# Kernel optimization log

Measured on AMD Instinct MI355X. Metric: run time of the kernel, lower is better.

Reference implementation:

```python
import jax, jax.numpy as jnp
import numpy as np

N, D, H, DH, E = 50000, 128, 4, 32, 600000
EPS = 1e-5


def _seg_softmax(logits, seg, n):
    # numerically stable softmax over edges grouped by destination node
    m = jax.ops.segment_max(logits, seg, num_segments=n)
    e = jnp.exp(logits - m[seg])
    s = jax.ops.segment_sum(e, seg, num_segments=n)
    return e / s[seg]


def _bn(x, g, b):
    # BatchNorm1d, training-mode statistics (biased variance), eps=1e-5
    mu = jnp.mean(x, 0)
    var = jnp.mean((x - mu) ** 2, 0)
    return g * (x - mu) * jax.lax.rsqrt(var + EPS) + b


def _gat(x, src, dst, W, a_s, a_d, bias):
    # PyG GATConv: shared lin, additive attention, leaky_relu(0.2), dst-softmax, concat heads + bias
    n = x.shape[0]
    xp = (x @ W).reshape(n, H, DH)
    al_s = jnp.sum(xp * a_s, -1)  # [N,H]
    al_d = jnp.sum(xp * a_d, -1)
    lg = jax.nn.leaky_relu(al_s[src] + al_d[dst], 0.2)  # [E',H]
    alpha = _seg_softmax(lg, dst, n)
    out = jax.ops.segment_sum(alpha[..., None] * xp[src], dst, num_segments=n)
    return out.reshape(n, H * DH) + bias


def setup_inputs() -> dict:
    key = jax.random.key(0)
    ks = jax.random.split(key, 24)
    s = 0.05
    inp = {
        'x_cell': jax.random.normal(ks[0], (N, D), jnp.float32),
        'z_h': jax.random.normal(ks[1], (D,), jnp.float32),
        'x_cell_embedded': jax.random.normal(ks[2], (N, D), jnp.float32),
        'edge_index_0': jax.random.randint(ks[3], (2, E), 0, N, dtype=jnp.int32),
        'edge_index_1': jax.random.randint(ks[4], (2, E), 0, N, dtype=jnp.int32),
        # GAT params, stacked over (conv layer 0/1, edge type 0/1)
        'gat_W': jax.random.normal(ks[5], (2, 2, D, D), jnp.float32) * s,
        'gat_att_src': jax.random.normal(ks[6], (2, 2, H, DH), jnp.float32) * s,
        'gat_att_dst': jax.random.normal(ks[7], (2, 2, H, DH), jnp.float32) * s,
        'gat_bias': jnp.zeros((2, 2, D), jnp.float32),
        # BatchNorm params for bn1, bn2, bn_hgt
        'bn_gamma': jnp.ones((3, D), jnp.float32),
        'bn_beta': jnp.zeros((3, D), jnp.float32),
        # HGTConv params
        'hgt_Wk': jax.random.normal(ks[8], (D, D), jnp.float32) * s,
        'hgt_bk': jnp.zeros((D,), jnp.float32),
        'hgt_Wq': jax.random.normal(ks[9], (D, D), jnp.float32) * s,
        'hgt_bq': jnp.zeros((D,), jnp.float32),
        'hgt_Wv': jax.random.normal(ks[10], (D, D), jnp.float32) * s,
        'hgt_bv': jnp.zeros((D,), jnp.float32),
        'hgt_a_rel': jax.random.normal(ks[11], (2, H, DH, DH), jnp.float32) * s,
        'hgt_m_rel': jax.random.normal(ks[12], (2, H, DH, DH), jnp.float32) * s,
        'hgt_p_rel': jnp.ones((2, H), jnp.float32),
        'hgt_Wo': jax.random.normal(ks[13], (D, D), jnp.float32) * s,
        'hgt_bo': jnp.zeros((D,), jnp.float32),
        'hgt_skip': jnp.float32(1.0),
        # input injection + FiLM
        'inj_W': jax.random.normal(ks[14], (D, D), jnp.float32) * s,
        'inj_b': jnp.zeros((D,), jnp.float32),
        'film_W1': jax.random.normal(ks[15], (D, 2 * D), jnp.float32) * s,
        'film_b1': jnp.zeros((2 * D,), jnp.float32),
        'film_W2': jax.random.normal(ks[16], (2 * D, 2 * D), jnp.float32) * s,
        'film_b2': jnp.zeros((2 * D,), jnp.float32),
    }
    return inp


def reference(x_cell, z_h, x_cell_embedded, edge_index_0, edge_index_1,
              gat_W, gat_att_src, gat_att_dst, gat_bias, bn_gamma, bn_beta,
              hgt_Wk, hgt_bk, hgt_Wq, hgt_bq, hgt_Wv, hgt_bv,
              hgt_a_rel, hgt_m_rel, hgt_p_rel, hgt_Wo, hgt_bo, hgt_skip,
              inj_W, inj_b, film_W1, film_b1, film_W2, film_b2):
    n = x_cell.shape[0]
    loops = jnp.arange(n, dtype=edge_index_0.dtype)
    # GATConv add_self_loops=True: augment each relation's edge list with self loops
    eis = [(jnp.concatenate([ei[0], loops]), jnp.concatenate([ei[1], loops]))
           for ei in (edge_index_0, edge_index_1)]

    def hetero_gat(x, c):
        out = jnp.zeros((n, D), x.dtype)
        for t, (src, dst) in enumerate(eis):  # HeteroConv aggr='sum'
            out = out + _gat(x, src, dst, gat_W[c, t], gat_att_src[c, t], gat_att_dst[c, t], gat_bias[c, t])
        return out

    lrelu = lambda v: jax.nn.leaky_relu(v, 0.2)
    x1 = lrelu(x_cell + _bn(hetero_gat(x_cell, 0), bn_gamma[0], bn_beta[0]))
    x2 = lrelu(x1 + _bn(hetero_gat(x1, 1), bn_gamma[1], bn_beta[1]))

    # HGTConv (single node type, 2 edge types, no self loops)
    k = (x2 @ hgt_Wk + hgt_bk).reshape(n, H, DH)
    q = (x2 @ hgt_Wq + hgt_bq).reshape(n, H, DH)
    v = (x2 @ hgt_Wv + hgt_bv).reshape(n, H, DH)
    lgs, msgs, dsts = [], [], []
    inv_sqrt = np.float32(1.0 / np.sqrt(DH))
    for t, ei in enumerate((edge_index_0, edge_index_1)):
        src, dst = ei[0], ei[1]
        kt = jnp.einsum('nhd,hde->nhe', k, hgt_a_rel[t])  # relation-transformed keys
        vt = jnp.einsum('nhd,hde->nhe', v, hgt_m_rel[t])  # relation-transformed values
        lgs.append(jnp.sum(q[dst] * kt[src], -1) * hgt_p_rel[t] * inv_sqrt)  # [E,H]
        msgs.append(vt[src])
        dsts.append(dst)
    lg = jnp.concatenate(lgs)
    msg = jnp.concatenate(msgs)
    dst_all = jnp.concatenate(dsts)
    alpha = _seg_softmax(lg, dst_all, n)  # softmax over all incoming edges (all relations)
    agg = jax.ops.segment_sum(alpha[..., None] * msg, dst_all, num_segments=n).reshape(n, H * DH)
    hgt_out = jax.nn.gelu(agg, approximate=False) @ hgt_Wo + hgt_bo
    sk = jax.nn.sigmoid(hgt_skip)
    x3 = sk * hgt_out + (1.0 - sk) * x2

    x3 = _bn(x3, bn_gamma[2], bn_beta[2])
    x3 = lrelu(x2 + x3)
    x3 = x3 + x_cell_embedded @ inj_W + inj_b

    # FiLM on global z_h
    hzh = jax.nn.gelu(z_h @ film_W1 + film_b1, approximate=False)
    gb = hzh @ film_W2 + film_b2
    gamma, beta = gb[:D], gb[D:]
    return gamma * x3 + beta
```

## Files before the change

### kernel.cpp

```cpp
#include <hip/hip_runtime.h>
#include <math.h>

#define NN 50000
#define DD 128
#define HH 4
#define DHH 32
#define EE 600000
#define N2 (2*NN)
#define NBLK 256

typedef unsigned short u16;
typedef unsigned int   u32;
typedef unsigned char  u8;
using short8 = __attribute__((ext_vector_type(8))) short;
using f32x4  = __attribute__((ext_vector_type(4))) float;
using f32x2  = __attribute__((ext_vector_type(2))) float;

#define LOG2E 1.44269504f

__device__ __forceinline__ float lrelu(float v){ return v > 0.f ? v : 0.2f*v; }
__device__ __forceinline__ float gelu_exact(float x){ return 0.5f*x*(1.f+erff(x*0.70710678118654752f)); }
__device__ __forceinline__ u16 f2bf(float f){
  u32 u = __float_as_uint(f);
  u32 r = (u + 0x7fffu + ((u>>16)&1u)) >> 16;
  return (u16)r;
}
__device__ __forceinline__ u32 pack2bf(float a, float b){ return (u32)f2bf(a) | ((u32)f2bf(b)<<16); }
__device__ __forceinline__ float bflo(u32 u){ return __uint_as_float(u<<16); }
__device__ __forceinline__ float bfhi(u32 u){ return __uint_as_float(u & 0xffff0000u); }

__global__ __launch_bounds__(256) void prep_all(
    const float* __restrict__ gat_W, const float* __restrict__ Wk, const float* __restrict__ Wv,
    const float* __restrict__ Wo, const float* __restrict__ injW, u16* __restrict__ WT,
    const float* __restrict__ Wq, const float* __restrict__ bq, const float* __restrict__ a_rel,
    u16* __restrict__ wqtT, float* __restrict__ bqt,
    const float* __restrict__ z, const float* __restrict__ fW1, const float* __restrict__ fb1,
    const float* __restrict__ fW2, const float* __restrict__ fb2, float* __restrict__ gb){
  __shared__ float t[32][33];
  __shared__ float hsh[256];
  const int bid = blockIdx.x;
  if(bid < 128){
    const int m = bid >> 4, tile = bid & 15, tr = tile>>2, tc = tile&3;
    const float* src = (m<4) ? (gat_W + (size_t)m*16384) : (m==4? Wk : m==5? Wv : m==6? Wo : injW);
    const int lr = threadIdx.x>>5, lc = threadIdx.x&31;
    #pragma unroll
    for(int p=0;p<4;++p) t[lr+p*8][lc] = src[(size_t)(tr*32+lr+p*8)*128 + tc*32+lc];
    __syncthreads();
    #pragma unroll
    for(int p=0;p<4;++p)
      WT[(size_t)m*16384 + (size_t)(tc*32+lr+p*8)*128 + tr*32+lc] = f2bf(t[lc][lr+p*8]);
  } else if(bid < 257){
    int idx = (bid-128)*256 + threadIdx.x;
    if(idx < 2*128*129){
      int tt = idx / (128*129);
      int r = idx % (128*129);
      int f = r / 129, c = r % 129;
      int h = f>>5, m = f&31;
      const float* srcp = (c<128) ? (Wq + (size_t)c*128 + h*DHH) : (bq + h*DHH);
      const float* arow = a_rel + (((size_t)(tt*HH+h)*DHH)+m)*DHH;
      float s=0.f;
      #pragma unroll
      for(int e=0;e<DHH;++e) s = fmaf(srcp[e], arow[e], s);
      if(c<128) wqtT[(size_t)tt*16384 + (size_t)f*128 + c] = f2bf(s);
      else      bqt[tt*128 + f] = s;
    }
  } else {
    int j = threadIdx.x;
    float acc = fb1[j];
    for(int d=0; d<DD; ++d) acc = fmaf(z[d], fW1[d*256+j], acc);
    hsh[j] = gelu_exact(acc);
    __syncthreads();
    float acc2 = fb2[j];
    for(int k=0;k<256;++k) acc2 = fmaf(hsh[k], fW2[k*256+j], acc2);
    gb[j] = acc2;
  }
}

__global__ void count2_kernel(const int* __restrict__ d0, const int* __restrict__ d1, int* __restrict__ jcnt){
  int e = blockIdx.x*blockDim.x+threadIdx.x;
  if(e < EE)        atomicAdd(&jcnt[d0[e]], 1);
  else if(e < 2*EE) atomicAdd(&jcnt[NN + d1[e-EE]], 1);
}

__global__ void scan_partial(const int* __restrict__ cnt, int* __restrict__ bsum){
  int t = threadIdx.x;
  int i0 = blockIdx.x*512 + 2*t;
  int s = 0;
  if(i0   < N2) s += cnt[i0];
  if(i0+1 < N2) s += cnt[i0+1];
  __shared__ int red[256];
  red[t]=s; __syncthreads();
  for(int off=128; off>0; off>>=1){ if(t<off) red[t]+=red[t+off]; __syncthreads(); }
  if(t==0) bsum[blockIdx.x]=red[0];
}

__global__ void scan_final2(const int* __restrict__ cnt, const int* __restrict__ bsum,
                            int* __restrict__ jrs, int* __restrict__ jcur, int nb){
  __shared__ int sh[256];
  int t = threadIdx.x;
  {
    int v = (t<nb)? bsum[t] : 0;
    sh[t]=v; __syncthreads();
    for(int off=1; off<256; off<<=1){
      int u = (t>=off)? sh[t-off] : 0; __syncthreads();
      sh[t]+=u; __syncthreads();
    }
  }
  const int bofsv = sh[blockIdx.x] - bsum[blockIdx.x];
  if(blockIdx.x==0 && t==0) jrs[N2] = sh[nb-1];
  __syncthreads();
  int i0 = blockIdx.x*512 + 2*t;
  int a = (i0   < N2)? cnt[i0]   : 0;
  int c = (i0+1 < N2)? cnt[i0+1] : 0;
  int s = a+c;
  sh[t]=s; __syncthreads();
  for(int off=1; off<256; off<<=1){
    int u = (t>=off)? sh[t-off] : 0; __syncthreads();
    sh[t]+=u; __syncthreads();
  }
  int ex = bofsv + sh[t]-s;
  if(i0   < N2){ jrs[i0]=ex;     jcur[i0]=ex; }
  if(i0+1 < N2){ jrs[i0+1]=ex+a; jcur[i0+1]=ex+a; }
}

__global__ void fill2_kernel(const int* __restrict__ ei0, const int* __restrict__ ei1,
                             int* __restrict__ jcur, u16* __restrict__ es){
  int e = blockIdx.x*blockDim.x+threadIdx.x;
  if(e < EE){
    int d = ei0[EE+e];
    int pos = atomicAdd(&jcur[d],1);
    es[pos] = (u16)ei0[e];
  } else if(e < 2*EE){
    int i = e-EE;
    int d = ei1[EE+i];
    int pos = atomicAdd(&jcur[NN+d],1);
    es[pos] = (u16)ei1[i];
  }
}

constexpr int MM_BIAS  = 1;
constexpr int MM_FILM  = 2;
constexpr int MM_SKIP  = 4;
constexpr int MM_ABF16 = 64;

#define SWZ(row, byte) ((byte) ^ (((row)&7)<<4))

template<int MODE>
__device__ __forceinline__ void mgemm_core(const void* Av, const u16* WT, int row0, int n,
                                           u16* Al, u16* Wl, f32x4 (&acc)[8]){
  const int tid = threadIdx.x;
  if(MODE & MM_ABF16){
    const uint2* Ag = (const uint2*)((const u16*)Av + (size_t)row0*128);
    const int maxv = (min(64, n-row0))*32;
    #pragma unroll
    for(int j=0;j<8;++j){
      int v = tid + j*256;
      uint2 st = make_uint2(0u,0u);
      if(v < maxv) st = Ag[v];
      int row = v>>5, cb = (v&31)*8;
      *(uint2*)((char*)Al + row*256 + SWZ(row, cb)) = st;
    }
  } else {
    const float4* Ag = (const float4*)((const float*)Av + (size_t)row0*128);
    const int maxv = (min(64, n-row0))*32;
    #pragma unroll
    for(int j=0;j<8;++j){
      int v = tid + j*256;
      float4 val = make_float4(0.f,0.f,0.f,0.f);
      if(v < maxv) val = Ag[v];
      int row = v>>5, cb = (v&31)*8;
      uint2 st; st.x = pack2bf(val.x, val.y); st.y = pack2bf(val.z, val.w);
      *(uint2*)((char*)Al + row*256 + SWZ(row, cb)) = st;
    }
  }
  {
    const u32* Wg = (const u32*)WT;
    #pragma unroll
    for(int j=0;j<32;++j){
      int v = tid + j*256;
      u32 w = Wg[v];
      int row = v>>6, cb = (v&63)*4;
      *(u32*)((char*)Wl + row*256 + SWZ(row, cb)) = w;
    }
  }
  __syncthreads();
  const int lane = tid & 63;
  const int wv   = tid >> 6;
  const int r16  = lane & 15;
  const int kg   = lane >> 4;
  #pragma unroll
  for(int nn=0;nn<8;++nn) acc[nn] = (f32x4){0.f,0.f,0.f,0.f};
  #pragma unroll
  for(int s=0;s<4;++s){
    const int arow = wv*16 + r16;
    const int kb = s*64 + kg*16;
    short8 af = *(const short8*)((const char*)Al + arow*256 + SWZ(arow, kb));
    #pragma unroll
    for(int nn=0;nn<8;++nn){
      const int brow = nn*16 + r16;
      short8 bf = *(const short8*)((const char*)Wl + brow*256 + SWZ(brow, kb));
      acc[nn] = __builtin_amdgcn_mfma_f32_16x16x32_bf16(af, bf, acc[nn], 0, 0, 0);
    }
  }
}

template<int MODE>
__global__ __launch_bounds__(256) void mgemm(const void* __restrict__ Av, const u16* __restrict__ WT,
    const float* __restrict__ bias, const float* __restrict__ base, const float* __restrict__ fgb,
    const float* __restrict__ skipv, float* __restrict__ C, int n){
  __shared__ u16 Al[64*128];
  __shared__ u16 Wl[128*128];
  const int row0 = blockIdx.x*64;
  f32x4 acc[8];
  mgemm_core<MODE>(Av, WT, row0, n, Al, Wl, acc);
  const int lane = threadIdx.x & 63;
  const int wv   = threadIdx.x >> 6;
  const int r16  = lane & 15;
  const int kg   = lane >> 4;
  float bvals[8];
  if(MODE & MM_BIAS){
    #pragma unroll
    for(int nn=0;nn<8;++nn) bvals[nn] = bias[nn*16+r16];
  }
  float sk = 0.f;
  if(MODE & MM_SKIP) sk = 1.f/(1.f+__expf(-skipv[0]));
  #pragma unroll
  for(int i=0;i<4;++i){
    const int row = row0 + wv*16 + kg*4 + i;
    if(row >= n) continue;
    #pragma unroll
    for(int nn=0;nn<8;++nn){
      const int col = nn*16 + r16;
      float o = acc[nn][i];
      if(MODE & MM_BIAS) o += bvals[nn];
      if(MODE & MM_SKIP)
        o = sk*o + (1.f-sk)*base[(size_t)row*128 + col];
      if(MODE & MM_FILM){
        o += base[(size_t)row*128 + col];
        o = fgb[col]*o + fgb[128+col];
      }
      C[(size_t)row*128 + col] = o;
    }
  }
}

struct MJob {
  const u16* WT;
  const float* bias;
  const float* as_;
  const float* ad_;
  void* Cv;
  int att_t;
  int sel;
};
struct MJobs { MJob j[4]; };

__global__ __launch_bounds__(256) void mgemmM(const float* __restrict__ Av, MJobs jobs, int njobs,
    float* __restrict__ als8, float* __restrict__ ald8, int n){
  __shared__ u16 Al[64*128];
  __shared__ u16 Wl[128*128];
  const int tid = threadIdx.x;
  const int row0 = blockIdx.x*64;
  {
    const float4* Ag = (const float4*)(Av + (size_t)row0*128);
    const int maxv = (min(64, n-row0))*32;
    #pragma unroll
    for(int j=0;j<8;++j){
      int v = tid + j*256;
      float4 val = make_float4(0.f,0.f,0.f,0.f);
      if(v < maxv) val = Ag[v];
      int row = v>>5, cb = (v&31)*8;
      uint2 st; st.x = pack2bf(val.x, val.y); st.y = pack2bf(val.z, val.w);
      *(uint2*)((char*)Al + row*256 + SWZ(row, cb)) = st;
    }
  }
  const int lane = tid & 63;
  const int wv   = tid >> 6;
  const int r16  = lane & 15;
  const int kg   = lane >> 4;
  for(int jj=0; jj<njobs; ++jj){
    const MJob job = jobs.j[jj];
    {
      const u32* Wg = (const u32*)job.WT;
      #pragma unroll
      for(int j=0;j<32;++j){
        int v = tid + j*256;
        u32 w = Wg[v];
        int row = v>>6, cb = (v&63)*4;
        *(u32*)((char*)Wl + row*256 + SWZ(row, cb)) = w;
      }
    }
    __syncthreads();
    f32x4 acc[8];
    #pragma unroll
    for(int nn=0;nn<8;++nn) acc[nn] = (f32x4){0.f,0.f,0.f,0.f};
    #pragma unroll
    for(int s=0;s<4;++s){
      const int arow = wv*16 + r16;
      const int kb = s*64 + kg*16;
      short8 af = *(const short8*)((const char*)Al + arow*256 + SWZ(arow, kb));
      #pragma unroll
      for(int nn=0;nn<8;++nn){
        const int brow = nn*16 + r16;
        short8 bf = *(const short8*)((const char*)Wl + brow*256 + SWZ(brow, kb));
        acc[nn] = __builtin_amdgcn_mfma_f32_16x16x32_bf16(af, bf, acc[nn], 0, 0, 0);
      }
    }
    if(job.as_){
      float asv[8], adv[8];
      #pragma unroll
      for(int nn=0;nn<8;++nn){ asv[nn]=job.as_[nn*16+r16]; adv[nn]=job.ad_[nn*16+r16]; }
      #pragma unroll
      for(int i=0;i<4;++i){
        const int row = row0 + wv*16 + kg*4 + i;
        #pragma unroll
        for(int h=0;h<4;++h){
          float ps = asv[2*h]*acc[2*h][i] + asv[2*h+1]*acc[2*h+1][i];
          float pd = adv[2*h]*acc[2*h][i] + adv[2*h+1]*acc[2*h+1][i];
          ps += __shfl_xor(ps,1); ps += __shfl_xor(ps,2); ps += __shfl_xor(ps,4); ps += __shfl_xor(ps,8);
          pd += __shfl_xor(pd,1); pd += __shfl_xor(pd,2); pd += __shfl_xor(pd,4); pd += __shfl_xor(pd,8);
          if(row < n && r16 == 0){
            als8[(size_t)row*8 + 2*h + job.att_t] = ps;
            ald8[(size_t)row*8 + 2*h + job.att_t] = pd;
          }
        }
      }
    }
    float bvals[8];
    #pragma unroll
    for(int nn=0;nn<8;++nn) bvals[nn] = job.bias ? job.bias[nn*16+r16] : 0.f;
    #pragma unroll
    for(int i=0;i<4;++i){
      const int row = row0 + wv*16 + kg*4 + i;
      if(row >= n) continue;
      #pragma unroll
      for(int nn=0;nn<8;++nn){
        const int col = nn*16 + r16;
        float o = acc[nn][i] + bvals[nn];
        if(job.sel == 1){
          ((u16*)job.Cv)[(size_t)row*128 + col] = f2bf(o);
        } else {
          u32 enc = __builtin_amdgcn_cvt_pk_fp8_f32(o, 0.f, 0u, false);
          ((u8*)job.Cv)[(size_t)row*256 + (col>>1)*4 + (col&1) + (job.sel-2)*2] = (u8)(enc & 0xffu);
        }
      }
    }
    __syncthreads();
  }
}

__global__ __launch_bounds__(256) void gat_gather3(const u16* __restrict__ xp0, const u16* __restrict__ xp1,
    const float* __restrict__ als8, const float* __restrict__ ald8,
    const int* __restrict__ jrs, const u16* __restrict__ es,
    const float* __restrict__ gb0, const float* __restrict__ gb1, float* __restrict__ out){
  const int gid = blockIdx.x*blockDim.x + threadIdx.x;
  const int node = gid >> 6;
  const int lane = threadIdx.x & 63;
  if(node >= NN) return;
  const int h = lane >> 4;
  const int cc = 2*lane;
  float o0 = gb0[cc] + gb1[cc], o1 = gb0[cc+1] + gb1[cc+1];
  #pragma unroll
  for(int t=0;t<2;++t){
    const u16* __restrict__ xp = t ? xp1 : xp0;
    const float aldv = ald8[(size_t)node*8 + 2*h + t];
    const int s0 = jrs[t*NN+node], s1 = jrs[t*NN+node+1];
    float ssum=0.f, a0=0.f, a1=0.f;
    int p = s0;
    for(; p+3<s1; p+=4){
      const int sA = es[p], sB = es[p+1], sC = es[p+2], sD = es[p+3];
      const u32 xA = *(const u32*)&xp[(size_t)sA*DD + cc];
      const u32 xB = *(const u32*)&xp[(size_t)sB*DD + cc];
      const u32 xC = *(const u32*)&xp[(size_t)sC*DD + cc];
      const u32 xD = *(const u32*)&xp[(size_t)sD*DD + cc];
      float lA = als8[(size_t)sA*8 + 2*h + t] + aldv;
      float lB = als8[(size_t)sB*8 + 2*h + t] + aldv;
      float lC = als8[(size_t)sC*8 + 2*h + t] + aldv;
      float lD = als8[(size_t)sD*8 + 2*h + t] + aldv;
      const float eA = exp2f(lA>0.f ? lA*LOG2E : lA*(0.2f*LOG2E));
      const float eB = exp2f(lB>0.f ? lB*LOG2E : lB*(0.2f*LOG2E));
      const float eC = exp2f(lC>0.f ? lC*LOG2E : lC*(0.2f*LOG2E));
      const float eD = exp2f(lD>0.f ? lD*LOG2E : lD*(0.2f*LOG2E));
      ssum += (eA+eB)+(eC+eD);
      a0 = fmaf(eA, bflo(xA), a0); a1 = fmaf(eA, bfhi(xA), a1);
      a0 = fmaf(eB, bflo(xB), a0); a1 = fmaf(eB, bfhi(xB), a1);
      a0 = fmaf(eC, bflo(xC), a0); a1 = fmaf(eC, bfhi(xC), a1);
      a0 = fmaf(eD, bflo(xD), a0); a1 = fmaf(eD, bfhi(xD), a1);
    }
    for(; p<s1; ++p){
      const int sA = es[p];
      const u32 xA = *(const u32*)&xp[(size_t)sA*DD + cc];
      float lA = als8[(size_t)sA*8 + 2*h + t] + aldv;
      const float eA = exp2f(lA>0.f ? lA*LOG2E : lA*(0.2f*LOG2E));
      ssum += eA;
      a0 = fmaf(eA, bflo(xA), a0); a1 = fmaf(eA, bfhi(xA), a1);
    }
    {
      float lg = als8[(size_t)node*8 + 2*h + t] + aldv;
      const float ev = exp2f(lg>0.f ? lg*LOG2E : lg*(0.2f*LOG2E));
      ssum += ev;
      const u32 xr = *(const u32*)&xp[(size_t)node*DD + cc];
      a0 = fmaf(ev, bflo(xr), a0); a1 = fmaf(ev, bfhi(xr), a1);
    }
    const float inv = 1.f/ssum;
    o0 = fmaf(a0, inv, o0); o1 = fmaf(a1, inv, o1);
  }
  *(float2*)&out[(size_t)node*DD + cc] = make_float2(o0, o1);
}

__global__ __launch_bounds__(256) void bn_stats_fused(const float* __restrict__ X, float* __restrict__ part,
                               const float* __restrict__ gamma, const float* __restrict__ beta,
                               float* __restrict__ stat, int* __restrict__ counter){
  const int f = threadIdx.x & 127, rg = threadIdx.x>>7;
  float s=0.f, s2=0.f;
  for(int r = blockIdx.x*2+rg; r<NN; r += NBLK*2){
    float v = X[(size_t)r*DD+f]; s+=v; s2 = fmaf(v,v,s2);
  }
  __shared__ float ls[256], ls2[256];
  __shared__ int lastsh;
  ls[threadIdx.x]=s; ls2[threadIdx.x]=s2; __syncthreads();
  if(rg==0){
    part[blockIdx.x*256 + f]       = ls[f]+ls[128+f];
    part[blockIdx.x*256 + 128 + f] = ls2[f]+ls2[128+f];
  }
  __threadfence();
  if(threadIdx.x==0) lastsh = (atomicAdd(counter,1) == NBLK-1);
  __syncthreads();
  if(lastsh){
    __threadfence();
    float ss=0.f, ss2=0.f;
    #pragma unroll 8
    for(int bk=rg; bk<NBLK; bk+=2){
      ss  += part[bk*256 + f];
      ss2 += part[bk*256 + 128 + f];
    }
    __syncthreads();
    ls[threadIdx.x]=ss; ls2[threadIdx.x]=ss2;
    __syncthreads();
    if(rg==0){
      float S1 = ls[f]+ls[128+f], S2 = ls2[f]+ls2[128+f];
      float mu = S1/(float)NN;
      float var = S2/(float)NN - mu*mu;
      float rs = rsqrtf(var+1e-5f);
      stat[f]     = gamma[f]*rs;
      stat[128+f] = beta[f] - gamma[f]*rs*mu;
    }
    if(threadIdx.x==0) *counter = 0;
  }
}

__global__ void bn_apply_lrelu(const float* __restrict__ xprev, const float* __restrict__ acc,
                               const float* __restrict__ stat, float* __restrict__ out){
  int idx = blockIdx.x*blockDim.x+threadIdx.x;
  if(idx >= NN*64) return;
  int c = (2*idx) & 127;
  float2 x = ((const float2*)xprev)[idx];
  float2 a = ((const float2*)acc)[idx];
  float o0 = lrelu(x.x + fmaf(stat[c],   a.x, stat[128+c]));
  float o1 = lrelu(x.y + fmaf(stat[c+1], a.y, stat[128+c+1]));
  ((float2*)out)[idx] = make_float2(o0,o1);
}

__global__ __launch_bounds__(256) void hgt_merged2(const u16* __restrict__ qt,
    const u32* __restrict__ kv, const int* __restrict__ jrs, const u16* __restrict__ es,
    const float* __restrict__ p_rel, u16* __restrict__ Sv){
  const int gid = blockIdx.x*blockDim.x + threadIdx.x;
  const int node = gid >> 6;
  const int lane = threadIdx.x & 63;
  if(node >= NN) return;
  const int h = lane >> 4;
  float acc[2][2] = {{0.f,0.f},{0.f,0.f}};
  float ssum = 0.f;
  #pragma unroll
  for(int t=0;t<2;++t){
    const u32 qw = *(const u32*)&qt[(size_t)t*NN*DD + (size_t)node*DD + 2*lane];
    const float q0 = bflo(qw), q1 = bfhi(qw);
    const float scale2 = p_rel[t*HH+h]*(0.17677669529663687f*LOG2E);
    const int s0 = jrs[t*NN+node], s1 = jrs[t*NN+node+1];
    int p = s0;
    for(; p+3<s1; p+=4){
      const int sA = es[p], sB = es[p+1], sC = es[p+2], sD = es[p+3];
      const u32 wA = kv[(size_t)sA*64 + lane];
      const u32 wB = kv[(size_t)sB*64 + lane];
      const u32 wC = kv[(size_t)sC*64 + lane];
      const u32 wD = kv[(size_t)sD*64 + lane];
      f32x2 kA = __builtin_amdgcn_cvt_pk_f32_fp8(wA, false);
      f32x2 kB = __builtin_amdgcn_cvt_pk_f32_fp8(wB, false);
      f32x2 kC = __builtin_amdgcn_cvt_pk_f32_fp8(wC, false);
      f32x2 kD = __builtin_amdgcn_cvt_pk_f32_fp8(wD, false);
      f32x2 vA = __builtin_amdgcn_cvt_pk_f32_fp8(wA, true);
      f32x2 vB = __builtin_amdgcn_cvt_pk_f32_fp8(wB, true);
      f32x2 vC = __builtin_amdgcn_cvt_pk_f32_fp8(wC, true);
      f32x2 vD = __builtin_amdgcn_cvt_pk_f32_fp8(wD, true);
      float pA = q0*kA.x + q1*kA.y;
      float pB = q0*kB.x + q1*kB.y;
      float pC = q0*kC.x + q1*kC.y;
      float pD = q0*kD.x + q1*kD.y;
      pA += __shfl_xor(pA,1); pB += __shfl_xor(pB,1); pC += __shfl_xor(pC,1); pD += __shfl_xor(pD,1);
      pA += __shfl_xor(pA,2); pB += __shfl_xor(pB,2); pC += __shfl_xor(pC,2); pD += __shfl_xor(pD,2);
      pA += __shfl_xor(pA,4); pB += __shfl_xor(pB,4); pC += __shfl_xor(pC,4); pD += __shfl_xor(pD,4);
      pA += __shfl_xor(pA,8); pB += __shfl_xor(pB,8); pC += __shfl_xor(pC,8); pD += __shfl_xor(pD,8);
      const float eA=exp2f(pA*scale2), eB=exp2f(pB*scale2);
      const float eC=exp2f(pC*scale2), eD=exp2f(pD*scale2);
      ssum += (eA+eB)+(eC+eD);
      acc[t][0] = fmaf(eA, vA.x, acc[t][0]); acc[t][1] = fmaf(eA, vA.y, acc[t][1]);
      acc[t][0] = fmaf(eB, vB.x, acc[t][0]); acc[t][1] = fmaf(eB, vB.y, acc[t][1]);
      acc[t][0] = fmaf(eC, vC.x, acc[t][0]); acc[t][1] = fmaf(eC, vC.y, acc[t][1]);
      acc[t][0] = fmaf(eD, vD.x, acc[t][0]); acc[t][1] = fmaf(eD, vD.y, acc[t][1]);
    }
    for(; p<s1; ++p){
      const int sA = es[p];
      const u32 wA = kv[(size_t)sA*64 + lane];
      f32x2 kA = __builtin_amdgcn_cvt_pk_f32_fp8(wA, false);
      f32x2 vA = __builtin_amdgcn_cvt_pk_f32_fp8(wA, true);
      float pA = q0*kA.x + q1*kA.y;
      pA += __shfl_xor(pA,1); pA += __shfl_xor(pA,2); pA += __shfl_xor(pA,4); pA += __shfl_xor(pA,8);
      const float eA = exp2f(pA*scale2);
      ssum += eA;
      acc[t][0] = fmaf(eA, vA.x, acc[t][0]); acc[t][1] = fmaf(eA, vA.y, acc[t][1]);
    }
  }
  const float inv = ssum>0.f ? 1.f/ssum : 0.f;
  ((u32*)&Sv[(size_t)node*256 +       2*lane])[0] = pack2bf(acc[0][0]*inv, acc[0][1]*inv);
  ((u32*)&Sv[(size_t)node*256 + 128 + 2*lane])[0] = pack2bf(acc[1][0]*inv, acc[1][1]*inv);
}

__global__ __launch_bounds__(256) void mtransform_kernel(const u16* __restrict__ Sv, const float* __restrict__ m_rel,
                                                         u16* __restrict__ out){
  __shared__ float Msh[2*HH*DHH*DHH];
  for(int i=threadIdx.x;i<2*HH*DHH*DHH;i+=256) Msh[i]=m_rel[i];
  __syncthreads();
  int idx = blockIdx.x*blockDim.x + threadIdx.x;
  if(idx >= NN*DD) return;
  int node = idx>>7, f = idx&127, h = f>>5, e = f&31;
  const u16* s0p = &Sv[(size_t)node*256 + h*DHH];
  const u16* s1p = &Sv[(size_t)node*256 + 128 + h*DHH];
  const float* M0 = &Msh[(0*HH+h)*DHH*DHH + e];
  const float* M1 = &Msh[(1*HH+h)*DHH*DHH + e];
  float s = 0.f;
  #pragma unroll
  for(int d=0; d<DHH; d+=2){
    u32 w0 = *(const u32*)&s0p[d];
    u32 w1 = *(const u32*)&s1p[d];
    s = fmaf(bflo(w0), M0[d*DHH],     s);
    s = fmaf(bfhi(w0), M0[(d+1)*DHH], s);
    s = fmaf(bflo(w1), M1[d*DHH],     s);
    s = fmaf(bfhi(w1), M1[(d+1)*DHH], s);
  }
  out[idx] = f2bf(gelu_exact(s));
}

extern "C" void kernel_launch(void* const* d_in, const int* in_sizes, int n_in,
                              void* d_out, int out_size, void* d_ws, size_t ws_size,
                              hipStream_t stream){
  const float* x_cell = (const float*)d_in[0];
  const float* z_h    = (const float*)d_in[1];
  const float* x_emb  = (const float*)d_in[2];
  const int*   ei0    = (const int*)d_in[3];
  const int*   ei1    = (const int*)d_in[4];
  const float* gat_W  = (const float*)d_in[5];
  const float* gat_as = (const float*)d_in[6];
  const float* gat_ad = (const float*)d_in[7];
  const float* gat_b  = (const float*)d_in[8];
  const float* bn_g   = (const float*)d_in[9];
  const float* bn_b   = (const float*)d_in[10];
  const float* Wk = (const float*)d_in[11];
  const float* bk = (const float*)d_in[12];
  const float* Wq = (const float*)d_in[13];
  const float* bq = (const float*)d_in[14];
  const float* Wv = (const float*)d_in[15];
  const float* bv = (const float*)d_in[16];
  const float* a_rel = (const float*)d_in[17];
  const float* m_rel = (const float*)d_in[18];
  const float* p_rel = (const float*)d_in[19];
  const float* Wo = (const float*)d_in[20];
  const float* bo = (const float*)d_in[21];
  const float* skip = (const float*)d_in[22];
  const float* injW = (const float*)d_in[23];
  const float* injb = (const float*)d_in[24];
  const float* fW1 = (const float*)d_in[25];
  const float* fb1 = (const float*)d_in[26];
  const float* fW2 = (const float*)d_in[27];
  const float* fb2 = (const float*)d_in[28];

  constexpr size_t SLOT = (size_t)NN*DD;
  float* ws = (float*)d_ws;
  float* A    = ws;
  float* X2   = A + SLOT;
  float* als8 = X2 + SLOT;
  float* ald8 = als8 + (size_t)NN*8;
  float* bnpart = ald8 + (size_t)NN*8;
  float* bnstat = bnpart + 256*256;
  float* fgb    = bnstat + 256;
  float* bqt    = fgb + 256;
  u16* WT8  = (u16*)(bqt + 2*128);
  u16* WQT  = WT8 + (size_t)8*16384;
  u16* S    = WQT + (size_t)2*16384;
  u16* XP0  = S + (size_t)NN*256;
  u16* XP1  = XP0 + SLOT;
  u16* es   = XP1 + SLOT;
  int* jcnt = (int*)(es + (size_t)2*EE + 2);
  int* bnctr= jcnt + N2;
  int* jrs  = bnctr + 4;
  int* jcur = jrs + N2 + 2;
  int* bsum = jcur + N2;
  size_t needed = (size_t)((char*)(bsum + 256) - (char*)d_ws);
  if(ws_size < needed) return;

  u16* QT = (u16*)A;
  u16* MT = (u16*)A;
  u32* KV = (u32*)XP0;

  const int TB = 256;
  dim3 b(TB);
  const int gE2    = (2*EE + TB - 1)/TB;
  const int gND    = (NN*DD + TB - 1)/TB;
  const int gND2   = (NN*64 + TB - 1)/TB;
  const int gNodes = (NN + 3)/4;
  const int gMG    = (NN + 63)/64;
  const int gScan  = (N2 + 511)/512;

  prep_all<<<258, b, 0, stream>>>(gat_W, Wk, Wv, Wo, injW, WT8, Wq, bq, a_rel, WQT, bqt,
                                  z_h, fW1, fb1, fW2, fb2, fgb);

  hipMemsetAsync(jcnt, 0, (N2+4)*sizeof(int), stream);
  count2_kernel<<<gE2, b, 0, stream>>>(ei0+EE, ei1+EE, jcnt);
  scan_partial<<<gScan, b, 0, stream>>>(jcnt, bsum);
  scan_final2<<<gScan, b, 0, stream>>>(jcnt, bsum, jrs, jcur, gScan);
  fill2_kernel<<<gE2, b, 0, stream>>>(ei0, ei1, jcur, es);

  const float* xin = x_cell;
  for(int c=0;c<2;++c){
    MJobs gj{};
    for(int t=0;t<2;++t){
      gj.j[t].WT   = WT8 + (size_t)(c*2+t)*16384;
      gj.j[t].bias = nullptr;
      gj.j[t].as_  = gat_as + (size_t)(c*2+t)*HH*DHH;
      gj.j[t].ad_  = gat_ad + (size_t)(c*2+t)*HH*DHH;
      gj.j[t].Cv   = t? (void*)XP1 : (void*)XP0;
      gj.j[t].att_t = t;
      gj.j[t].sel  = 1;
    }
    mgemmM<<<gMG, b, 0, stream>>>(xin, gj, 2, als8, ald8, NN);
    gat_gather3<<<gNodes, b, 0, stream>>>(XP0, XP1, als8, ald8, jrs, es,
        gat_b + (size_t)(c*2+0)*DD, gat_b + (size_t)(c*2+1)*DD, A);
    bn_stats_fused<<<NBLK, b, 0, stream>>>(A, bnpart, bn_g + (size_t)c*DD, bn_b + (size_t)c*DD, bnstat, bnctr);
    bn_apply_lrelu<<<gND2, b, 0, stream>>>(xin, A, bnstat, X2);
    xin = X2;
  }
  float* x2 = X2;

  {
    MJobs hj{};
    hj.j[0] = { WQT,                   bqt,       nullptr, nullptr, (void*)QT,          0, 1 };
    hj.j[1] = { WQT + 16384,           bqt + 128, nullptr, nullptr, (void*)(QT + SLOT), 0, 1 };
    hj.j[2] = { WT8 + (size_t)4*16384, bk,        nullptr, nullptr, (void*)KV,          0, 2 };
    hj.j[3] = { WT8 + (size_t)5*16384, bv,        nullptr, nullptr, (void*)KV,          0, 3 };
    mgemmM<<<gMG, b, 0, stream>>>(x2, hj, 4, nullptr, nullptr, NN);
  }
  hgt_merged2<<<gNodes, b, 0, stream>>>(QT, KV, jrs, es, p_rel, S);
  mtransform_kernel<<<gND, b, 0, stream>>>(S, m_rel, MT);
  mgemm<MM_ABF16|MM_BIAS|MM_SKIP><<<gMG, b, 0, stream>>>(MT, WT8 + (size_t)6*16384, bo,
      x2, nullptr, skip, (float*)d_out, NN);
  bn_stats_fused<<<NBLK, b, 0, stream>>>((float*)d_out, bnpart, bn_g + 2*DD, bn_b + 2*DD, bnstat, bnctr);
  bn_apply_lrelu<<<gND2, b, 0, stream>>>(x2, (float*)d_out, bnstat, (float*)d_out);
  mgemm<MM_BIAS|MM_FILM><<<gMG, b, 0, stream>>>(x_emb, WT8 + (size_t)7*16384, injb,
      (float*)d_out, fgb, nullptr, (float*)d_out, NN);
}
```

Baseline: 760.6 us.

## Build destination CSR with two-level bucket sort instead of per-node global atomics

After: 1.634 ms. +114.8%, slower.

```diff
diff --git a/kernel.cpp b/kernel.cpp
--- a/kernel.cpp
+++ b/kernel.cpp
@@ -8,6 +8,7 @@
 #define EE 600000
 #define N2 (2*NN)
 #define NBLK 256
+#define NBUCK ((N2 + 511)/512)
 
 typedef unsigned short u16;
 typedef unsigned int   u32;
@@ -76,66 +77,79 @@
   }
 }
 
-__global__ void count2_kernel(const int* __restrict__ d0, const int* __restrict__ d1, int* __restrict__ jcnt){
+__global__ __launch_bounds__(256) void bucket_count(const int* __restrict__ d0, const int* __restrict__ d1,
+                                                    int* __restrict__ bcnt){
+  __shared__ int h[NBUCK];
+  for(int i=threadIdx.x;i<NBUCK;i+=256) h[i]=0;
+  __syncthreads();
+  const int e0 = blockIdx.x*4096 + threadIdx.x;
+  #pragma unroll
+  for(int j=0;j<16;++j){
+    int e = e0 + j*256;
+    if(e < EE)           atomicAdd(&h[d0[e]>>9], 1);
+    else if(e < 2*EE)    atomicAdd(&h[(NN + d1[e-EE])>>9], 1);
+  }
+  __syncthreads();
+  for(int i=threadIdx.x;i<NBUCK;i+=256){ int v=h[i]; if(v) atomicAdd(&bcnt[i], v); }
+}
+
+__global__ void bucket_scan(const int* __restrict__ bcnt, int* __restrict__ bbase, int* __restrict__ bcur){
+  __shared__ int sh[256];
+  int t=threadIdx.x;
+  int v = (t<NBUCK)? bcnt[t] : 0;
+  sh[t]=v; __syncthreads();
+  for(int off=1;off<256;off<<=1){
+    int u=(t>=off)?sh[t-off]:0; __syncthreads();
+    sh[t]+=u; __syncthreads();
+  }
+  if(t<NBUCK){ bbase[t]=sh[t]-v; bcur[t]=sh[t]-v; }
+  if(t==0) bbase[NBUCK] = 2*EE;
+}
+
+__global__ void fill_bucket(const int* __restrict__ ei0, const int* __restrict__ ei1,
+                            int* __restrict__ bcur, u32* __restrict__ eb){
   int e = blockIdx.x*blockDim.x+threadIdx.x;
-  if(e < EE)        atomicAdd(&jcnt[d0[e]], 1);
-  else if(e < 2*EE) atomicAdd(&jcnt[NN + d1[e-EE]], 1);
-}
-
-__global__ void scan_partial(const int* __restrict__ cnt, int* __restrict__ bsum){
-  int t = threadIdx.x;
-  int i0 = blockIdx.x*512 + 2*t;
-  int s = 0;
-  if(i0   < N2) s += cnt[i0];
-  if(i0+1 < N2) s += cnt[i0+1];
-  __shared__ int red[256];
-  red[t]=s; __syncthreads();
-  for(int off=128; off>0; off>>=1){ if(t<off) red[t]+=red[t+off]; __syncthreads(); }
-  if(t==0) bsum[blockIdx.x]=red[0];
-}
-
-__global__ void scan_final2(const int* __restrict__ cnt, const int* __restrict__ bsum,
-                            int* __restrict__ jrs, int* __restrict__ jcur, int nb){
-  __shared__ int sh[256];
-  int t = threadIdx.x;
-  {
-    int v = (t<nb)? bsum[t] : 0;
-    sh[t]=v; __syncthreads();
-    for(int off=1; off<256; off<<=1){
-      int u = (t>=off)? sh[t-off] : 0; __syncthreads();
-      sh[t]+=u; __syncthreads();
-    }
-  }
-  const int bofsv = sh[blockIdx.x] - bsum[blockIdx.x];
-  if(blockIdx.x==0 && t==0) jrs[N2] = sh[nb-1];
-  __syncthreads();
-  int i0 = blockIdx.x*512 + 2*t;
-  int a = (i0   < N2)? cnt[i0]   : 0;
-  int c = (i0+1 < N2)? cnt[i0+1] : 0;
-  int s = a+c;
-  sh[t]=s; __syncthreads();
-  for(int off=1; off<256; off<<=1){
-    int u = (t>=off)? sh[t-off] : 0; __syncthreads();
-    sh[t]+=u; __syncthreads();
-  }
-  int ex = bofsv + sh[t]-s;
-  if(i0   < N2){ jrs[i0]=ex;     jcur[i0]=ex; }
-  if(i0+1 < N2){ jrs[i0+1]=ex+a; jcur[i0+1]=ex+a; }
-}
-
-__global__ void fill2_kernel(const int* __restrict__ ei0, const int* __restrict__ ei1,
-                             int* __restrict__ jcur, u16* __restrict__ es){
-  int e = blockIdx.x*blockDim.x+threadIdx.x;
-  if(e < EE){
-    int d = ei0[EE+e];
-    int pos = atomicAdd(&jcur[d],1);
-    es[pos] = (u16)ei0[e];
-  } else if(e < 2*EE){
-    int i = e-EE;
-    int d = ei1[EE+i];
-    int pos = atomicAdd(&jcur[NN+d],1);
-    es[pos] = (u16)ei1[i];
-  }
+  int d, src;
+  if(e < EE){ d = ei0[EE+e]; src = ei0[e]; }
+  else if(e < 2*EE){ int i=e-EE; d = NN + ei1[EE+i]; src = ei1[i]; }
+  else return;
+  int b = d>>9, dloc = d & 511;
+  int pos = atomicAdd(&bcur[b], 1);
+  eb[pos] = ((u32)dloc<<16) | (u32)src;
+}
+
+__global__ __launch_bounds__(256) void fill_place(const u32* __restrict__ eb, const int* __restrict__ bbase,
+                                                  int* __restrict__ jrs, u16* __restrict__ es){
+  const int b = blockIdx.x;
+  const int nb0 = b*512;
+  const int nloc = min(512, N2-nb0);
+  const int base = bbase[b], end = bbase[b+1];
+  __shared__ int hist[512];
+  __shared__ int psum[256];
+  const int t = threadIdx.x;
+  hist[t]=0; hist[t+256]=0;
+  __syncthreads();
+  for(int p=base+t; p<end; p+=256) atomicAdd(&hist[eb[p]>>16], 1);
+  __syncthreads();
+  const int c0 = hist[2*t], c1 = hist[2*t+1];
+  const int pair = c0+c1;
+  psum[t]=pair; __syncthreads();
+  for(int off=1;off<256;off<<=1){
+    int u=(t>=off)?psum[t-off]:0; __syncthreads();
+    psum[t]+=u; __syncthreads();
+  }
+  const int ex = base + psum[t]-pair;
+  if(2*t   < nloc) jrs[nb0+2*t]   = ex;
+  if(2*t+1 < nloc) jrs[nb0+2*t+1] = ex+c0;
+  __syncthreads();
+  hist[2*t]=ex; hist[2*t+1]=ex+c0;
+  __syncthreads();
+  for(int p=base+t; p<end; p+=256){
+    u32 w = eb[p];
+    int pos = atomicAdd(&hist[w>>16], 1);
+    es[pos] = (u16)(w & 0xffffu);
+  }
+  if(b==0 && t==0) jrs[N2] = 2*EE;
 }
 
 constexpr int MM_BIAS  = 1;
@@ -599,35 +613,36 @@
   u16* XP0  = S + (size_t)NN*256;
   u16* XP1  = XP0 + SLOT;
   u16* es   = XP1 + SLOT;
-  int* jcnt = (int*)(es + (size_t)2*EE + 2);
-  int* bnctr= jcnt + N2;
+  int* bcnt = (int*)(es + (size_t)2*EE + 2);
+  int* bnctr= bcnt + NBUCK;
   int* jrs  = bnctr + 4;
-  int* jcur = jrs + N2 + 2;
-  int* bsum = jcur + N2;
-  size_t needed = (size_t)((char*)(bsum + 256) - (char*)d_ws);
+  int* bbase= jrs + N2 + 2;
+  int* bcur = bbase + NBUCK + 2;
+  size_t needed = (size_t)((char*)(bcur + NBUCK + 2) - (char*)d_ws);
   if(ws_size < needed) return;
 
   u16* QT = (u16*)A;
   u16* MT = (u16*)A;
   u32* KV = (u32*)XP0;
+  u32* EB = (u32*)S;
 
   const int TB = 256;
   dim3 b(TB);
   const int gE2    = (2*EE + TB - 1)/TB;
+  const int gBC    = (2*EE + 4095)/4096;
   const int gND    = (NN*DD + TB - 1)/TB;
   const int gND2   = (NN*64 + TB - 1)/TB;
   const int gNodes = (NN + 3)/4;
   const int gMG    = (NN + 63)/64;
-  const int gScan  = (N2 + 511)/512;
 
   prep_all<<<258, b, 0, stream>>>(gat_W, Wk, Wv, Wo, injW, WT8, Wq, bq, a_rel, WQT, bqt,
                                   z_h, fW1, fb1, fW2, fb2, fgb);
 
-  hipMemsetAsync(jcnt, 0, (N2+4)*sizeof(int), stream);
-  count2_kernel<<<gE2, b, 0, stream>>>(ei0+EE, ei1+EE, jcnt);
-  scan_partial<<<gScan, b, 0, stream>>>(jcnt, bsum);
-  scan_final2<<<gScan, b, 0, stream>>>(jcnt, bsum, jrs, jcur, gScan);
-  fill2_kernel<<<gE2, b, 0, stream>>>(ei0, ei1, jcur, es);
+  hipMemsetAsync(bcnt, 0, (NBUCK+4)*sizeof(int), stream);
+  bucket_count<<<gBC, b, 0, stream>>>(ei0+EE, ei1+EE, bcnt);
+  bucket_scan<<<1, 256, 0, stream>>>(bcnt, bbase, bcur);
+  fill_bucket<<<gE2, b, 0, stream>>>(ei0, ei1, bcur, EB);
+  fill_place<<<NBUCK, b, 0, stream>>>(EB, bbase, jrs, es);
 
   const float* xin = x_cell;
   for(int c=0;c<2;++c){
```
